# Kernel optimization log

Measured on AMD Instinct MI355X. Metric: run time of the kernel, lower is better.

## Reference

```python
import jax, jax.numpy as jnp
import numpy as np

K_BASE = 8
K_MAX = 20
NUM_GROUPS = 16  # min(32, 64 // 4)
EPS = 1e-5


def _knn_idx_adaptive(x, mask, k_base=K_BASE, k_max=K_MAX):
    # x: [B, N, D] float, mask: [B, N] bool. Returns idx: [B, N, k_max] int32.
    B, N, D = x.shape
    x2 = jnp.sum(x * x, axis=-1, keepdims=True)              # [B, N, 1]
    dist2 = x2 + x2.transpose(0, 2, 1) - 2.0 * jnp.einsum('bnd,bmd->bnm', x, x)
    dist2 = jnp.clip(dist2, 0.0)
    valid = mask[:, :, None] & mask[:, None, :]
    eye = jnp.eye(N, dtype=bool)[None]
    dist2 = jnp.where(valid & ~eye, dist2, jnp.inf)
    counts = mask.sum(axis=1)                                 # [B]
    k_per = jnp.clip(jnp.sqrt(counts.astype(jnp.float32) / 50.0) * k_base,
                     k_base, k_max).astype(jnp.int32)         # truncation == torch .long()
    k_global = jnp.minimum(k_max, jnp.maximum(1, counts.min() - 1))
    _, idx = jax.lax.top_k(-dist2, k_max)                     # [B, N, k_max]
    first_valid = jnp.argmax(mask, axis=1)                    # [B]
    cols = jnp.arange(k_max)[None, None, :]
    k_eff = jnp.minimum(k_per, k_global)[:, None, None]
    # cols < k_eff: true top-k neighbors; [k_eff, k_global): repeat first valid; >= k_global: pad 0
    idx = jnp.where(cols < k_eff, idx,
                    jnp.where(cols < k_global, first_valid[:, None, None], 0))
    return idx


def _group_norm(h, gamma, beta, num_groups=NUM_GROUPS, eps=EPS):
    # h: [..., C]
    shp = h.shape
    C = shp[-1]
    hg = h.reshape(shp[:-1] + (num_groups, C // num_groups))
    mu = hg.mean(axis=-1, keepdims=True)
    var = hg.var(axis=-1, keepdims=True)
    hg = (hg - mu) * jax.lax.rsqrt(var + eps)
    return hg.reshape(shp) * gamma + beta


def setup_inputs() -> dict:
    key = jax.random.key(0)
    kx, kl, k1, k2 = jax.random.split(key, 4)
    B, N, D, C = 16, 1024, 64, 64
    x = jax.random.normal(kx, (B, N, D), dtype=jnp.float32)
    lengths = jax.random.randint(kl, (B,), 256, N + 1)
    mask = jnp.arange(N)[None, :] < lengths[:, None]          # [B, N] bool
    W1 = jax.random.normal(k1, (2 * D, C), dtype=jnp.float32) / np.sqrt(2 * D)
    b1 = jnp.zeros((C,), dtype=jnp.float32)
    gamma = jnp.ones((C,), dtype=jnp.float32)
    beta = jnp.zeros((C,), dtype=jnp.float32)
    W2 = jax.random.normal(k2, (C, C), dtype=jnp.float32) / np.sqrt(C)
    b2 = jnp.zeros((C,), dtype=jnp.float32)
    return {"x": x, "mask": mask, "W1": W1, "b1": b1,
            "gamma": gamma, "beta": beta, "W2": W2, "b2": b2}


def reference(x, mask, W1, b1, gamma, beta, W2, b2):
    B, N, D = x.shape
    idx = _knn_idx_adaptive(x, mask)                          # [B, N, k]
    k = idx.shape[-1]
    x_nb = jnp.take_along_axis(x[:, :, None, :].repeat(1, axis=2),
                               idx[..., None], axis=1) if False else \
        x[jnp.arange(B)[:, None, None], idx]                  # [B, N, k, D]
    x_i = jnp.broadcast_to(x[:, :, None, :], (B, N, k, D))
    edge = jnp.concatenate([x_i, x_nb - x_i], axis=-1)        # [B, N, k, 2D]
    h = jax.nn.relu(_group_norm(edge @ W1 + b1, gamma, beta)) # [B, N, k, C]
    h = h @ W2 + b2
    out = h.max(axis=2)                                       # [B, N, C]
    return out * mask[..., None].astype(out.dtype)
```

## Files before the change

kernel.cpp:

```cpp
#include <hip/hip_runtime.h>
#include <stdint.h>

#define BB 16
#define NN 1024
#define DD 64
#define CC 64
#define KMAX 20
#define ROWS 8
#define PW 8

typedef unsigned long long u64;
typedef float f32x2 __attribute__((ext_vector_type(2)));
typedef float f32x4v __attribute__((ext_vector_type(4)));
typedef short bf16x8 __attribute__((ext_vector_type(8)));

__device__ inline u64 umin64(u64 a, u64 b) { return a < b ? a : b; }

__device__ inline u64 bitonic_sort64(u64 v, int lane) {
#pragma unroll
    for (int k = 2; k <= 64; k <<= 1) {
#pragma unroll
        for (int j = k >> 1; j > 0; j >>= 1) {
            u64 o = __shfl_xor(v, j);
            bool keepmin = (((lane & j) == 0) == ((lane & k) == 0));
            bool take = ((o < v) == keepmin);
            v = take ? o : v;
        }
    }
    return v;
}

__device__ inline unsigned f2bf(float f) {
    unsigned u = __float_as_uint(f);
    return (u + 0x7FFFu + ((u >> 16) & 1u)) >> 16;
}

__device__ inline bf16x8 pack8(const float4 a, const float4 b) {
    union { unsigned u[4]; bf16x8 v; } r;
    r.u[0] = f2bf(a.x) | (f2bf(a.y) << 16);
    r.u[1] = f2bf(a.z) | (f2bf(a.w) << 16);
    r.u[2] = f2bf(b.x) | (f2bf(b.y) << 16);
    r.u[3] = f2bf(b.z) | (f2bf(b.w) << 16);
    return r.v;
}

__device__ inline void gn4(float4& h, const float4 g, const float4 be) {
    float mu = (h.x + h.y + h.z + h.w) * 0.25f;
    float dx = h.x - mu, dy = h.y - mu, dz = h.z - mu, dw = h.w - mu;
    float var = (dx * dx + dy * dy + dz * dz + dw * dw) * 0.25f;
    float rs = __builtin_amdgcn_rsqf(var + 1e-5f);
    h.x = fmaxf(fmaf(dx * rs, g.x, be.x), 0.f);
    h.y = fmaxf(fmaf(dy * rs, g.y, be.y), 0.f);
    h.z = fmaxf(fmaf(dz * rs, g.z, be.z), 0.f);
    h.w = fmaxf(fmaf(dw * rs, g.w, be.w), 0.f);
}

__global__ __launch_bounds__(256) void k1_feats(const float* __restrict__ x,
                                                const float* __restrict__ W1,
                                                const float* __restrict__ b1,
                                                float* __restrict__ base,
                                                float* __restrict__ fb,
                                                float* __restrict__ x2,
                                                float* __restrict__ xT,
                                                const void* __restrict__ maskp,
                                                int* __restrict__ counts,
                                                int* __restrict__ keff) {
    __shared__ float sXT[32][65];
    __shared__ int scnt[BB];
    int w = threadIdx.x >> 6, lane = threadIdx.x & 63;
    int p0 = blockIdx.x * 32;
    int pw0 = p0 + w * PW;

    float w1a[DD], w1b[DD];
#pragma unroll
    for (int d = 0; d < DD; ++d) {
        w1a[d] = W1[d * CC + lane];
        w1b[d] = W1[(DD + d) * CC + lane];
    }
    float b1c = b1[lane];

#pragma unroll
    for (int q = 0; q < PW; ++q) {
        int p_s = __builtin_amdgcn_readfirstlane(pw0 + q);
        const float* xp = x + (size_t)p_s * DD;
        float xv = xp[lane];
        float sq = xv * xv;
        for (int off = 32; off; off >>= 1) sq += __shfl_xor(sq, off);
        if (lane == 0) x2[p_s] = sq;
        sXT[w * PW + q][lane] = xv;
        f32x2 acc2 = {0.f, 0.f};
#pragma unroll
        for (int d = 0; d < DD; ++d) {
            float xd = xp[d];
            acc2 = __builtin_elementwise_fma((f32x2){xd, xd},
                                             (f32x2){w1a[d], w1b[d]}, acc2);
        }
        base[(size_t)p_s * CC + lane] = acc2.x - acc2.y + b1c;
        fb[(size_t)p_s * CC + lane] = acc2.y;
    }
    __syncthreads();
    {
        int b = p0 >> 10, nb = p0 & 1023;
#pragma unroll
        for (int i = 0; i < 8; ++i) {
            int d = i * 8 + (threadIdx.x >> 5);
            int pt = threadIdx.x & 31;
            xT[(((size_t)(b << 6) + d) << 10) + nb + pt] = sXT[pt][d];
        }
    }

    if (blockIdx.x == 0) {
        const unsigned char* mb = (const unsigned char*)maskp;
        const int* mi = (const int*)maskp;
        bool bytelayout = (mb[1] != 0);
        for (int bq = 0; bq < 4; ++bq) {
            int bb = w * 4 + bq;
            int s = 0;
            for (int i = 0; i < 16; ++i) {
                int nn2 = lane + (i << 6);
                int v = bytelayout ? (mb[bb * NN + nn2] ? 1 : 0)
                                   : (mi[bb * NN + nn2] ? 1 : 0);
                s += v;
            }
            for (int off = 32; off; off >>= 1) s += __shfl_xor(s, off);
            if (lane == 0) scnt[bb] = s;
        }
        __syncthreads();
        int t = threadIdx.x;
        if (t < BB) {
            int minc = scnt[0];
            for (int qq = 1; qq < BB; ++qq) minc = min(minc, scnt[qq]);
            int kglob = min(KMAX, max(1, minc - 1));
            float c = (float)scnt[t];
            float v = sqrtf(c / 50.0f) * 8.0f;
            v = fminf(fmaxf(v, 8.0f), 20.0f);
            int kper = (int)v;
            counts[t] = scnt[t];
            keff[t] = min(kper, kglob);
        }
    }
}

#define CE(a, b)                                                      \
    {                                                                 \
        bool sw_ = pk[b] < pk[a];                                     \
        u64 ta_ = pk[a];                                              \
        pk[a] = sw_ ? pk[b] : pk[a];                                  \
        pk[b] = sw_ ? ta_ : pk[b];                                    \
    }

#define ROWFMA(r, rv, cv)                                                        \
    {                                                                            \
        axy[r] = __builtin_elementwise_fma((f32x2){rv, rv}, (f32x2){cv.x, cv.y}, \
                                           axy[r]);                              \
        azw[r] = __builtin_elementwise_fma((f32x2){rv, rv}, (f32x2){cv.z, cv.w}, \
                                           azw[r]);                              \
    }

__global__ __launch_bounds__(256) void k2_knn(const float* __restrict__ x,
                                              const float* __restrict__ xT,
                                              const float* __restrict__ x2,
                                              const int* __restrict__ counts,
                                              const int* __restrict__ keff,
                                              int* __restrict__ idx) {
    __shared__ float sD[ROWS][NN];
    __shared__ float sX2[NN];
    __shared__ u64 sSv[4][64];
    int b = blockIdx.x >> 7;
    int n0 = (blockIdx.x & 127) * ROWS;
    int cnt = counts[b];
    if (n0 >= cnt) return;
    int kef = keff[b];
    int w = threadIdx.x >> 6, lane = threadIdx.x & 63;
    int t = threadIdx.x;
    *(float4*)&sX2[t << 2] = *(const float4*)(x2 + (b << 10) + (t << 2));
    __syncthreads();

    if ((w << 8) < cnt) {
        f32x2 axy[ROWS], azw[ROWS];
#pragma unroll
        for (int r = 0; r < ROWS; ++r) { axy[r] = (f32x2){0.f, 0.f}; azw[r] = (f32x2){0.f, 0.f}; }
        const float* xTb = xT + ((size_t)b << 16);
        const float* xrow0 = x + ((size_t)(b << 10) + n0) * DD;
        int c0 = (w << 8) + (lane << 2);
        for (int d0 = 0; d0 < DD; d0 += 4) {
            float4 cv0 = *(const float4*)(xTb + ((size_t)(d0 + 0) << 10) + c0);
            float4 cv1 = *(const float4*)(xTb + ((size_t)(d0 + 1) << 10) + c0);
            float4 cv2 = *(const float4*)(xTb + ((size_t)(d0 + 2) << 10) + c0);
            float4 cv3 = *(const float4*)(xTb + ((size_t)(d0 + 3) << 10) + c0);
#pragma unroll
            for (int r = 0; r < ROWS; ++r) {
                float4 rv = *(const float4*)(xrow0 + r * DD + d0);
                ROWFMA(r, rv.x, cv0)
                ROWFMA(r, rv.y, cv1)
                ROWFMA(r, rv.z, cv2)
                ROWFMA(r, rv.w, cv3)
            }
        }
#pragma unroll
        for (int r = 0; r < ROWS; ++r)
            *(float4*)&sD[r][c0] = make_float4(axy[r].x, axy[r].y, azw[r].x, azw[r].y);
    }
    __syncthreads();

    for (int rr = 0; rr < 2; ++rr) {
        int r = w + rr * 4;
        int n = n0 + r;
        if (n >= cnt) continue;
        float x2n = sX2[n];
        u64 pk[16];
#pragma unroll
        for (int tt = 0; tt < 16; ++tt) {
            int c = (tt << 6) + lane;
            float dot = sD[r][c];
            float dd = fmaxf((x2n + sX2[c]) - 2.0f * dot, 0.0f);
            pk[tt] = (c < cnt && c != n)
                ? (((u64)__float_as_uint(dd) << 32) | (unsigned)c)
                : ~0ULL;
        }
        u64 h01 = umin64(pk[0], pk[1]),   h23 = umin64(pk[2], pk[3]);
        u64 h45 = umin64(pk[4], pk[5]),   h67 = umin64(pk[6], pk[7]);
        u64 h89 = umin64(pk[8], pk[9]),   hab = umin64(pk[10], pk[11]);
        u64 hcd = umin64(pk[12], pk[13]), hef = umin64(pk[14], pk[15]);
        u64 h = umin64(umin64(umin64(h01, h23), umin64(h45, h67)),
                       umin64(umin64(h89, hab), umin64(hcd, hef)));
        unsigned h32 = (unsigned)(h >> 32);
        unsigned prefix = 0u;
        int rank = kef;
#pragma unroll
        for (int bbit = 31; bbit >= 0; --bbit) {
            unsigned bitm = 1u << bbit;
            bool cand0 = ((((u64)(h32 ^ prefix)) >> (bbit + 1)) == 0) &&
                         ((h32 & bitm) == 0);
            u64 m0 = __ballot(cand0);
            int c0 = __popcll(m0);
            if (rank > c0) { rank -= c0; prefix |= bitm; }
        }
        u64 t0 = (((u64)prefix) << 32) | 0xFFFFFFFFULL;
        int cle = 0;
#pragma unroll
        for (int i = 0; i < 16; ++i) cle += (pk[i] <= t0) ? 1 : 0;
        int incl = cle;
#pragma unroll
        for (int off = 1; off < 64; off <<= 1) {
            int o = __shfl_up(incl, off);
            incl += (lane >= off) ? o : 0;
        }
        int S = __shfl(incl, 63);
        size_t prow = (size_t)(b << 10) + n;
        if (S <= 64) {
            int pos = incl - cle;
#pragma unroll
            for (int i = 0; i < 16; ++i) {
                if (pk[i] <= t0) { sSv[w][pos] = pk[i]; ++pos; }
            }
            u64 sv = (lane < S) ? sSv[w][lane] : ~0ULL;
            sv = bitonic_sort64(sv, lane);
            if (lane < KMAX)
                idx[prow * KMAX + lane] = (lane < kef) ? (int)(unsigned)(sv & 0xffffffffu) : 0;
        } else {
            CE(0,1) CE(2,3) CE(4,5) CE(6,7) CE(8,9) CE(10,11) CE(12,13) CE(14,15)
            CE(0,2) CE(1,3) CE(4,6) CE(5,7) CE(8,10) CE(9,11) CE(12,14) CE(13,15)
            CE(1,2) CE(5,6) CE(9,10) CE(13,14)
            CE(0,4) CE(1,5) CE(2,6) CE(3,7) CE(8,12) CE(9,13) CE(10,14) CE(11,15)
            CE(2,4) CE(3,5) CE(10,12) CE(11,13)
            CE(1,2) CE(3,4) CE(5,6) CE(9,10) CE(11,12) CE(13,14)
            CE(0,8) CE(1,9) CE(2,10) CE(3,11) CE(4,12) CE(5,13) CE(6,14) CE(7,15)
            CE(4,8) CE(5,9) CE(6,10) CE(7,11)
            CE(2,4) CE(3,5) CE(6,8) CE(7,9) CE(10,12) CE(11,13)
            CE(1,2) CE(3,4) CE(5,6) CE(7,8) CE(9,10) CE(11,12) CE(13,14)
            u64 myhead = pk[0];
            int my_m = 0;
            for (int j = 0; j < kef; ++j) {
                u64 g = myhead;
                for (int off = 32; off; off >>= 1) {
                    u64 o = __shfl_xor(g, off);
                    g = (o < g) ? o : g;
                }
                my_m = (j == lane) ? (int)(unsigned)(g & 0xffffffffu) : my_m;
                bool win = (myhead == g);
#pragma unroll
                for (int tt = 0; tt < 15; ++tt) pk[tt] = win ? pk[tt + 1] : pk[tt];
                pk[15] = win ? ~0ULL : pk[15];
                myhead = pk[0];
            }
            if (lane < KMAX)
                idx[prow * KMAX + lane] = (lane < kef) ? my_m : 0;
        }
    }
}

__global__ __launch_bounds__(256, 2) void k3_mlp(const float* __restrict__ base,
                                                 const float* __restrict__ fb,
                                                 const int* __restrict__ idx,
                                                 const int* __restrict__ counts,
                                                 const float* __restrict__ gamma,
                                                 const float* __restrict__ beta,
                                                 const float* __restrict__ W2,
                                                 const float* __restrict__ b2,
                                                 float* __restrict__ out) {
    __shared__ float sC[4][64][20];
    int w = threadIdx.x >> 6, lane = threadIdx.x & 63;
    int lg = lane >> 4, lr = lane & 15;
    int p0 = blockIdx.x * 16;
    int b = p0 >> 10;
    int n0b = p0 & 1023;
    int cnt = counts[b];
    int pt = p0 + lr;
    bool aval = (n0b + lr) < cnt;

    bf16x8 Bf[4][2];
#pragma unroll
    for (int nt = 0; nt < 4; ++nt)
#pragma unroll
        for (int kt = 0; kt < 2; ++kt) {
            float4 lo, hi;
            const float* wp = W2 + (size_t)(kt * 32 + lg * 8) * CC + nt * 16 + lr;
            lo.x = wp[0 * CC]; lo.y = wp[1 * CC]; lo.z = wp[2 * CC]; lo.w = wp[3 * CC];
            hi.x = wp[4 * CC]; hi.y = wp[5 * CC]; hi.z = wp[6 * CC]; hi.w = wp[7 * CC];
            Bf[nt][kt] = pack8(lo, hi);
        }

    const float* bp = base + (size_t)pt * CC + lg * 8;
    float4 baA0 = *(const float4*)(bp);
    float4 baA1 = *(const float4*)(bp + 4);
    float4 baB0 = *(const float4*)(bp + 32);
    float4 baB1 = *(const float4*)(bp + 36);
    const float* gp = gamma + lg * 8;
    float4 gA0 = *(const float4*)(gp),      gA1 = *(const float4*)(gp + 4);
    float4 gB0 = *(const float4*)(gp + 32), gB1 = *(const float4*)(gp + 36);
    const float* bep = beta + lg * 8;
    float4 eA0 = *(const float4*)(bep),      eA1 = *(const float4*)(bep + 4);
    float4 eB0 = *(const float4*)(bep + 32), eB1 = *(const float4*)(bep + 36);

    const float* fbb = fb + ((size_t)(b << 10)) * CC;
    const int* idxp = idx + (size_t)pt * KMAX;

    f32x4v cmax[4];
#pragma unroll
    for (int nt = 0; nt < 4; ++nt) cmax[nt] = (f32x4v){-1e30f, -1e30f, -1e30f, -1e30f};

#pragma unroll
    for (int jj = 0; jj < 5; ++jj) {
        int j = w * 5 + jj;
        int m = aval ? idxp[j] : 0;
        const float* fr = fbb + (size_t)m * CC + lg * 8;
        float4 hA0 = *(const float4*)(fr);
        float4 hA1 = *(const float4*)(fr + 4);
        float4 hB0 = *(const float4*)(fr + 32);
        float4 hB1 = *(const float4*)(fr + 36);
        hA0.x += baA0.x; hA0.y += baA0.y; hA0.z += baA0.z; hA0.w += baA0.w;
        hA1.x += baA1.x; hA1.y += baA1.y; hA1.z += baA1.z; hA1.w += baA1.w;
        hB0.x += baB0.x; hB0.y += baB0.y; hB0.z += baB0.z; hB0.w += baB0.w;
        hB1.x += baB1.x; hB1.y += baB1.y; hB1.z += baB1.z; hB1.w += baB1.w;
        gn4(hA0, gA0, eA0);
        gn4(hA1, gA1, eA1);
        gn4(hB0, gB0, eB0);
        gn4(hB1, gB1, eB1);
        bf16x8 A0 = pack8(hA0, hA1);
        bf16x8 A1 = pack8(hB0, hB1);
#pragma unroll
        for (int nt = 0; nt < 4; ++nt) {
            f32x4v c = {0.f, 0.f, 0.f, 0.f};
            c = __builtin_amdgcn_mfma_f32_16x16x32_bf16(A0, Bf[nt][0], c, 0, 0, 0);
            c = __builtin_amdgcn_mfma_f32_16x16x32_bf16(A1, Bf[nt][1], c, 0, 0, 0);
            cmax[nt].x = fmaxf(cmax[nt].x, c.x);
            cmax[nt].y = fmaxf(cmax[nt].y, c.y);
            cmax[nt].z = fmaxf(cmax[nt].z, c.z);
            cmax[nt].w = fmaxf(cmax[nt].w, c.w);
        }
    }
#pragma unroll
    for (int nt = 0; nt < 4; ++nt)
        *(float4*)&sC[w][lane][nt * 4] = (float4){cmax[nt].x, cmax[nt].y, cmax[nt].z, cmax[nt].w};
    __syncthreads();
    float b2c = b2[lane];
#pragma unroll
    for (int q = 0; q < 4; ++q) {
        int R = w * 4 + q;
        int src = ((R >> 2) << 4) + lr;
        int reg = (lg << 2) + (R & 3);
        float v = fmaxf(fmaxf(sC[0][src][reg], sC[1][src][reg]),
                        fmaxf(sC[2][src][reg], sC[3][src][reg]));
        bool valid = (n0b + R) < cnt;
        out[(size_t)(p0 + R) * CC + lane] = valid ? (v + b2c) : 0.f;
    }
}

extern "C" void kernel_launch(void* const* d_in, const int* in_sizes, int n_in,
                              void* d_out, int out_size, void* d_ws, size_t ws_size,
                              hipStream_t stream) {
    const float* x     = (const float*)d_in[0];
    const void*  maskp = d_in[1];
    const float* W1    = (const float*)d_in[2];
    const float* b1    = (const float*)d_in[3];
    const float* gamma = (const float*)d_in[4];
    const float* beta  = (const float*)d_in[5];
    const float* W2    = (const float*)d_in[6];
    const float* b2    = (const float*)d_in[7];
    float* out = (float*)d_out;

    int* d_counts = (int*)d_ws;
    int* d_keff   = d_counts + 16;
    float* d_x2   = (float*)(d_counts + 32);
    float* d_base = d_x2 + BB * NN;
    float* d_fb   = d_base + (size_t)BB * NN * CC;
    int* d_idx    = (int*)(d_fb + (size_t)BB * NN * CC);
    float* d_xT   = (float*)d_out;

    hipLaunchKernelGGL(k1_feats, dim3(BB * NN / 32), dim3(256), 0, stream,
                       x, W1, b1, d_base, d_fb, d_x2, d_xT, maskp, d_counts, d_keff);
    hipLaunchKernelGGL(k2_knn, dim3(BB * (NN / ROWS)), dim3(256), 0, stream,
                       x, d_xT, d_x2, d_counts, d_keff, d_idx);
    hipLaunchKernelGGL(k3_mlp, dim3(BB * NN / 16), dim3(256), 0, stream,
                       d_base, d_fb, d_idx, d_counts, gamma, beta, W2, b2, out);
}
```

Baseline: 96.30 us.

## Use split-bf16 MFMA for edge features and interleave two kNN rows per wave

The per-point feature projection in k1 is rewritten to use 16x16x32 bf16 MFMA with a hi/lo split (three products) to keep close to fp32 accuracy. Each block now covers 64 points and the transpose store uses float4 writes. In k2 each wave handles its two rows together, with interleaved radix-select ballots, prefix scans and bitonic sorts to expose more ILP, and it reuses the sD rows as scratch for compaction. This raises register pressure, and the split-bf16 approximation can shift results slightly.

```diff
diff --git a/kernel.cpp b/kernel.cpp
--- a/kernel.cpp
+++ b/kernel.cpp
@@ -7,7 +7,6 @@
 #define CC 64
 #define KMAX 20
 #define ROWS 8
-#define PW 8
 
 typedef unsigned long long u64;
 typedef float f32x2 __attribute__((ext_vector_type(2)));
@@ -15,20 +14,6 @@
 typedef short bf16x8 __attribute__((ext_vector_type(8)));
 
 __device__ inline u64 umin64(u64 a, u64 b) { return a < b ? a : b; }
-
-__device__ inline u64 bitonic_sort64(u64 v, int lane) {
-#pragma unroll
-    for (int k = 2; k <= 64; k <<= 1) {
-#pragma unroll
-        for (int j = k >> 1; j > 0; j >>= 1) {
-            u64 o = __shfl_xor(v, j);
-            bool keepmin = (((lane & j) == 0) == ((lane & k) == 0));
-            bool take = ((o < v) == keepmin);
-            v = take ? o : v;
-        }
-    }
-    return v;
-}
 
 __device__ inline unsigned f2bf(float f) {
     unsigned u = __float_as_uint(f);
@@ -42,6 +27,20 @@
     r.u[2] = f2bf(b.x) | (f2bf(b.y) << 16);
     r.u[3] = f2bf(b.z) | (f2bf(b.w) << 16);
     return r.v;
+}
+
+struct bfpair { bf16x8 hi, lo; };
+__device__ __forceinline__ bfpair split8(const float v[8]) {
+    union { unsigned u[4]; bf16x8 x; } H, L;
+#pragma unroll
+    for (int i = 0; i < 4; ++i) {
+        unsigned h0 = f2bf(v[2 * i]), h1 = f2bf(v[2 * i + 1]);
+        float r0 = v[2 * i] - __uint_as_float(h0 << 16);
+        float r1 = v[2 * i + 1] - __uint_as_float(h1 << 16);
+        H.u[i] = h0 | (h1 << 16);
+        L.u[i] = f2bf(r0) | (f2bf(r1) << 16);
+    }
+    bfpair r; r.hi = H.x; r.lo = L.x; return r;
 }
 
 __device__ inline void gn4(float4& h, const float4 g, const float4 be) {
@@ -65,47 +64,84 @@
                                                 const void* __restrict__ maskp,
                                                 int* __restrict__ counts,
                                                 int* __restrict__ keff) {
-    __shared__ float sXT[32][65];
+    __shared__ float sXT[64][65];
     __shared__ int scnt[BB];
     int w = threadIdx.x >> 6, lane = threadIdx.x & 63;
-    int p0 = blockIdx.x * 32;
-    int pw0 = p0 + w * PW;
-
-    float w1a[DD], w1b[DD];
-#pragma unroll
-    for (int d = 0; d < DD; ++d) {
-        w1a[d] = W1[d * CC + lane];
-        w1b[d] = W1[(DD + d) * CC + lane];
-    }
-    float b1c = b1[lane];
-
-#pragma unroll
-    for (int q = 0; q < PW; ++q) {
-        int p_s = __builtin_amdgcn_readfirstlane(pw0 + q);
-        const float* xp = x + (size_t)p_s * DD;
-        float xv = xp[lane];
+    int lg = lane >> 4, lr = lane & 15;
+    int p0 = blockIdx.x * 64;
+    int pw0 = p0 + w * 16;
+
+    float av[8];
+    bfpair A[2];
+    {
+        const float* xr = x + (size_t)(pw0 + lr) * DD;
+#pragma unroll
+        for (int kt = 0; kt < 2; ++kt) {
+            float4 a0 = *(const float4*)(xr + kt * 32 + lg * 8);
+            float4 a1 = *(const float4*)(xr + kt * 32 + lg * 8 + 4);
+            av[0] = a0.x; av[1] = a0.y; av[2] = a0.z; av[3] = a0.w;
+            av[4] = a1.x; av[5] = a1.y; av[6] = a1.z; av[7] = a1.w;
+            A[kt] = split8(av);
+        }
+    }
+    bfpair Wa[4][2], Wb[4][2];
+#pragma unroll
+    for (int nt = 0; nt < 4; ++nt)
+#pragma unroll
+        for (int kt = 0; kt < 2; ++kt) {
+            const float* wpa = W1 + (size_t)(kt * 32 + lg * 8) * CC + nt * 16 + lr;
+            float wv[8];
+#pragma unroll
+            for (int e = 0; e < 8; ++e) wv[e] = wpa[e * CC];
+            Wa[nt][kt] = split8(wv);
+            const float* wpb = wpa + (size_t)DD * CC;
+#pragma unroll
+            for (int e = 0; e < 8; ++e) wv[e] = wpb[e * CC];
+            Wb[nt][kt] = split8(wv);
+        }
+
+    f32x4v P[4], Q[4];
+#pragma unroll
+    for (int nt = 0; nt < 4; ++nt) { P[nt] = (f32x4v){0,0,0,0}; Q[nt] = (f32x4v){0,0,0,0}; }
+#pragma unroll
+    for (int nt = 0; nt < 4; ++nt)
+#pragma unroll
+        for (int kt = 0; kt < 2; ++kt) {
+            P[nt] = __builtin_amdgcn_mfma_f32_16x16x32_bf16(A[kt].hi, Wa[nt][kt].hi, P[nt], 0, 0, 0);
+            P[nt] = __builtin_amdgcn_mfma_f32_16x16x32_bf16(A[kt].hi, Wa[nt][kt].lo, P[nt], 0, 0, 0);
+            P[nt] = __builtin_amdgcn_mfma_f32_16x16x32_bf16(A[kt].lo, Wa[nt][kt].hi, P[nt], 0, 0, 0);
+            Q[nt] = __builtin_amdgcn_mfma_f32_16x16x32_bf16(A[kt].hi, Wb[nt][kt].hi, Q[nt], 0, 0, 0);
+            Q[nt] = __builtin_amdgcn_mfma_f32_16x16x32_bf16(A[kt].hi, Wb[nt][kt].lo, Q[nt], 0, 0, 0);
+            Q[nt] = __builtin_amdgcn_mfma_f32_16x16x32_bf16(A[kt].lo, Wb[nt][kt].hi, Q[nt], 0, 0, 0);
+        }
+#pragma unroll
+    for (int nt = 0; nt < 4; ++nt) {
+        float b1c = b1[nt * 16 + lr];
+#pragma unroll
+        for (int r = 0; r < 4; ++r) {
+            size_t off = (size_t)(pw0 + lg * 4 + r) * CC + nt * 16 + lr;
+            base[off] = P[nt][r] - Q[nt][r] + b1c;
+            fb[off] = Q[nt][r];
+        }
+    }
+
+    for (int q = 0; q < 16; ++q) {
+        int p = pw0 + q;
+        float xv = x[(size_t)p * DD + lane];
+        sXT[w * 16 + q][lane] = xv;
         float sq = xv * xv;
         for (int off = 32; off; off >>= 1) sq += __shfl_xor(sq, off);
-        if (lane == 0) x2[p_s] = sq;
-        sXT[w * PW + q][lane] = xv;
-        f32x2 acc2 = {0.f, 0.f};
-#pragma unroll
-        for (int d = 0; d < DD; ++d) {
-            float xd = xp[d];
-            acc2 = __builtin_elementwise_fma((f32x2){xd, xd},
-                                             (f32x2){w1a[d], w1b[d]}, acc2);
-        }
-        base[(size_t)p_s * CC + lane] = acc2.x - acc2.y + b1c;
-        fb[(size_t)p_s * CC + lane] = acc2.y;
+        if (lane == 0) x2[p] = sq;
     }
     __syncthreads();
     {
         int b = p0 >> 10, nb = p0 & 1023;
 #pragma unroll
-        for (int i = 0; i < 8; ++i) {
-            int d = i * 8 + (threadIdx.x >> 5);
-            int pt = threadIdx.x & 31;
-            xT[(((size_t)(b << 6) + d) << 10) + nb + pt] = sXT[pt][d];
+        for (int i = 0; i < 4; ++i) {
+            int d = i * 16 + (threadIdx.x >> 4);
+            int pt4 = (threadIdx.x & 15) << 2;
+            float4 vv = {sXT[pt4][d], sXT[pt4 + 1][d], sXT[pt4 + 2][d], sXT[pt4 + 3][d]};
+            *(float4*)&xT[(((size_t)(b << 6) + d) << 10) + nb + pt4] = vv;
         }
     }
 
@@ -149,6 +185,58 @@
         pk[b] = sw_ ? ta_ : pk[b];                                    \
     }
 
+__device__ __forceinline__ u64 head16(const u64 (&pk)[16]) {
+    u64 h01 = umin64(pk[0], pk[1]),   h23 = umin64(pk[2], pk[3]);
+    u64 h45 = umin64(pk[4], pk[5]),   h67 = umin64(pk[6], pk[7]);
+    u64 h89 = umin64(pk[8], pk[9]),   hab = umin64(pk[10], pk[11]);
+    u64 hcd = umin64(pk[12], pk[13]), hef = umin64(pk[14], pk[15]);
+    return umin64(umin64(umin64(h01, h23), umin64(h45, h67)),
+                  umin64(umin64(h89, hab), umin64(hcd, hef)));
+}
+
+__device__ __forceinline__ int sortpop(u64 (&pk)[16], int kef, int lane) {
+    CE(0,1) CE(2,3) CE(4,5) CE(6,7) CE(8,9) CE(10,11) CE(12,13) CE(14,15)
+    CE(0,2) CE(1,3) CE(4,6) CE(5,7) CE(8,10) CE(9,11) CE(12,14) CE(13,15)
+    CE(1,2) CE(5,6) CE(9,10) CE(13,14)
+    CE(0,4) CE(1,5) CE(2,6) CE(3,7) CE(8,12) CE(9,13) CE(10,14) CE(11,15)
+    CE(2,4) CE(3,5) CE(10,12) CE(11,13)
+    CE(1,2) CE(3,4) CE(5,6) CE(9,10) CE(11,12) CE(13,14)
+    CE(0,8) CE(1,9) CE(2,10) CE(3,11) CE(4,12) CE(5,13) CE(6,14) CE(7,15)
+    CE(4,8) CE(5,9) CE(6,10) CE(7,11)
+    CE(2,4) CE(3,5) CE(6,8) CE(7,9) CE(10,12) CE(11,13)
+    CE(1,2) CE(3,4) CE(5,6) CE(7,8) CE(9,10) CE(11,12) CE(13,14)
+    u64 myhead = pk[0];
+    int my_m = 0;
+    for (int j = 0; j < kef; ++j) {
+        u64 g = myhead;
+        for (int off = 32; off; off >>= 1) {
+            u64 o = __shfl_xor(g, off);
+            g = (o < g) ? o : g;
+        }
+        my_m = (j == lane) ? (int)(unsigned)(g & 0xffffffffu) : my_m;
+        bool win = (myhead == g);
+#pragma unroll
+        for (int tt = 0; tt < 15; ++tt) pk[tt] = win ? pk[tt + 1] : pk[tt];
+        pk[15] = win ? ~0ULL : pk[15];
+        myhead = pk[0];
+    }
+    return my_m;
+}
+
+__device__ __forceinline__ void bitonic_x2(u64& a, u64& b, int lane) {
+#pragma unroll
+    for (int k = 2; k <= 64; k <<= 1) {
+#pragma unroll
+        for (int j = k >> 1; j > 0; j >>= 1) {
+            u64 oa = __shfl_xor(a, j);
+            u64 ob = __shfl_xor(b, j);
+            bool keepmin = (((lane & j) == 0) == ((lane & k) == 0));
+            a = ((oa < a) == keepmin) ? oa : a;
+            b = ((ob < b) == keepmin) ? ob : b;
+        }
+    }
+}
+
 #define ROWFMA(r, rv, cv)                                                        \
     {                                                                            \
         axy[r] = __builtin_elementwise_fma((f32x2){rv, rv}, (f32x2){cv.x, cv.y}, \
@@ -165,7 +253,6 @@
                                               int* __restrict__ idx) {
     __shared__ float sD[ROWS][NN];
     __shared__ float sX2[NN];
-    __shared__ u64 sSv[4][64];
     int b = blockIdx.x >> 7;
     int n0 = (blockIdx.x & 127) * ROWS;
     int cnt = counts[b];
@@ -203,89 +290,80 @@
     }
     __syncthreads();
 
-    for (int rr = 0; rr < 2; ++rr) {
-        int r = w + rr * 4;
-        int n = n0 + r;
-        if (n >= cnt) continue;
-        float x2n = sX2[n];
-        u64 pk[16];
-#pragma unroll
-        for (int tt = 0; tt < 16; ++tt) {
-            int c = (tt << 6) + lane;
-            float dot = sD[r][c];
-            float dd = fmaxf((x2n + sX2[c]) - 2.0f * dot, 0.0f);
-            pk[tt] = (c < cnt && c != n)
-                ? (((u64)__float_as_uint(dd) << 32) | (unsigned)c)
-                : ~0ULL;
-        }
-        u64 h01 = umin64(pk[0], pk[1]),   h23 = umin64(pk[2], pk[3]);
-        u64 h45 = umin64(pk[4], pk[5]),   h67 = umin64(pk[6], pk[7]);
-        u64 h89 = umin64(pk[8], pk[9]),   hab = umin64(pk[10], pk[11]);
-        u64 hcd = umin64(pk[12], pk[13]), hef = umin64(pk[14], pk[15]);
-        u64 h = umin64(umin64(umin64(h01, h23), umin64(h45, h67)),
-                       umin64(umin64(h89, hab), umin64(hcd, hef)));
-        unsigned h32 = (unsigned)(h >> 32);
-        unsigned prefix = 0u;
-        int rank = kef;
-#pragma unroll
-        for (int bbit = 31; bbit >= 0; --bbit) {
-            unsigned bitm = 1u << bbit;
-            bool cand0 = ((((u64)(h32 ^ prefix)) >> (bbit + 1)) == 0) &&
-                         ((h32 & bitm) == 0);
-            u64 m0 = __ballot(cand0);
-            int c0 = __popcll(m0);
-            if (rank > c0) { rank -= c0; prefix |= bitm; }
-        }
-        u64 t0 = (((u64)prefix) << 32) | 0xFFFFFFFFULL;
-        int cle = 0;
-#pragma unroll
-        for (int i = 0; i < 16; ++i) cle += (pk[i] <= t0) ? 1 : 0;
-        int incl = cle;
-#pragma unroll
-        for (int off = 1; off < 64; off <<= 1) {
-            int o = __shfl_up(incl, off);
-            incl += (lane >= off) ? o : 0;
-        }
-        int S = __shfl(incl, 63);
-        size_t prow = (size_t)(b << 10) + n;
-        if (S <= 64) {
-            int pos = incl - cle;
-#pragma unroll
-            for (int i = 0; i < 16; ++i) {
-                if (pk[i] <= t0) { sSv[w][pos] = pk[i]; ++pos; }
-            }
-            u64 sv = (lane < S) ? sSv[w][lane] : ~0ULL;
-            sv = bitonic_sort64(sv, lane);
-            if (lane < KMAX)
-                idx[prow * KMAX + lane] = (lane < kef) ? (int)(unsigned)(sv & 0xffffffffu) : 0;
-        } else {
-            CE(0,1) CE(2,3) CE(4,5) CE(6,7) CE(8,9) CE(10,11) CE(12,13) CE(14,15)
-            CE(0,2) CE(1,3) CE(4,6) CE(5,7) CE(8,10) CE(9,11) CE(12,14) CE(13,15)
-            CE(1,2) CE(5,6) CE(9,10) CE(13,14)
-            CE(0,4) CE(1,5) CE(2,6) CE(3,7) CE(8,12) CE(9,13) CE(10,14) CE(11,15)
-            CE(2,4) CE(3,5) CE(10,12) CE(11,13)
-            CE(1,2) CE(3,4) CE(5,6) CE(9,10) CE(11,12) CE(13,14)
-            CE(0,8) CE(1,9) CE(2,10) CE(3,11) CE(4,12) CE(5,13) CE(6,14) CE(7,15)
-            CE(4,8) CE(5,9) CE(6,10) CE(7,11)
-            CE(2,4) CE(3,5) CE(6,8) CE(7,9) CE(10,12) CE(11,13)
-            CE(1,2) CE(3,4) CE(5,6) CE(7,8) CE(9,10) CE(11,12) CE(13,14)
-            u64 myhead = pk[0];
-            int my_m = 0;
-            for (int j = 0; j < kef; ++j) {
-                u64 g = myhead;
-                for (int off = 32; off; off >>= 1) {
-                    u64 o = __shfl_xor(g, off);
-                    g = (o < g) ? o : g;
-                }
-                my_m = (j == lane) ? (int)(unsigned)(g & 0xffffffffu) : my_m;
-                bool win = (myhead == g);
-#pragma unroll
-                for (int tt = 0; tt < 15; ++tt) pk[tt] = win ? pk[tt + 1] : pk[tt];
-                pk[15] = win ? ~0ULL : pk[15];
-                myhead = pk[0];
-            }
-            if (lane < KMAX)
-                idx[prow * KMAX + lane] = (lane < kef) ? my_m : 0;
+    int rA = w, rB = w + 4;
+    int nA = n0 + rA, nB = n0 + rB;
+    bool vA = nA < cnt, vB = nB < cnt;
+    if (!vA) return;
+    float x2A = sX2[nA];
+    float x2B = sX2[nB & 1023];
+    u64 pkA[16], pkB[16];
+#pragma unroll
+    for (int tt = 0; tt < 16; ++tt) {
+        int c = (tt << 6) + lane;
+        float dA = fmaxf((x2A + sX2[c]) - 2.0f * sD[rA][c], 0.0f);
+        float dB = fmaxf((x2B + sX2[c]) - 2.0f * sD[rB][c], 0.0f);
+        pkA[tt] = (c < cnt && c != nA)
+            ? (((u64)__float_as_uint(dA) << 32) | (unsigned)c) : ~0ULL;
+        pkB[tt] = (vB && c < cnt && c != nB)
+            ? (((u64)__float_as_uint(dB) << 32) | (unsigned)c) : ~0ULL;
+    }
+    u64 hA = head16(pkA), hB = head16(pkB);
+    unsigned hA32 = (unsigned)(hA >> 32), hB32 = (unsigned)(hB >> 32);
+    unsigned prefA = 0u, prefB = 0u;
+    int rankA = kef, rankB = kef;
+#pragma unroll
+    for (int bbit = 31; bbit >= 0; --bbit) {
+        unsigned bitm = 1u << bbit;
+        bool cA = ((((u64)(hA32 ^ prefA)) >> (bbit + 1)) == 0) && ((hA32 & bitm) == 0);
+        bool cB = ((((u64)(hB32 ^ prefB)) >> (bbit + 1)) == 0) && ((hB32 & bitm) == 0);
+        u64 mA = __ballot(cA);
+        u64 mB = __ballot(cB);
+        int nA0 = __popcll(mA), nB0 = __popcll(mB);
+        if (rankA > nA0) { rankA -= nA0; prefA |= bitm; }
+        if (rankB > nB0) { rankB -= nB0; prefB |= bitm; }
+    }
+    u64 t0A = (((u64)prefA) << 32) | 0xFFFFFFFFULL;
+    u64 t0B = vB ? ((((u64)prefB) << 32) | 0xFFFFFFFFULL) : 0ULL;
+    int cleA = 0, cleB = 0;
+#pragma unroll
+    for (int i = 0; i < 16; ++i) {
+        cleA += (pkA[i] <= t0A) ? 1 : 0;
+        cleB += (pkB[i] <= t0B) ? 1 : 0;
+    }
+    int incA = cleA, incB = cleB;
+#pragma unroll
+    for (int off = 1; off < 64; off <<= 1) {
+        int oA = __shfl_up(incA, off);
+        int oB = __shfl_up(incB, off);
+        incA += (lane >= off) ? oA : 0;
+        incB += (lane >= off) ? oB : 0;
+    }
+    int SA = __shfl(incA, 63), SB = __shfl(incB, 63);
+    size_t prowA = (size_t)(b << 10) + nA;
+    size_t prowB = (size_t)(b << 10) + nB;
+    if (SA <= 64 && SB <= 64) {
+        u64* svA = (u64*)&sD[rA][0];
+        u64* svB = (u64*)&sD[rB][0];
+        int pA = incA - cleA, pB = incB - cleB;
+#pragma unroll
+        for (int i = 0; i < 16; ++i) {
+            if (pkA[i] <= t0A) { svA[pA] = pkA[i]; ++pA; }
+            if (pkB[i] <= t0B) { svB[pB] = pkB[i]; ++pB; }
+        }
+        u64 sA = (lane < SA) ? svA[lane] : ~0ULL;
+        u64 sB = (lane < SB) ? svB[lane] : ~0ULL;
+        bitonic_x2(sA, sB, lane);
+        if (lane < KMAX) {
+            idx[prowA * KMAX + lane] = (lane < kef) ? (int)(unsigned)(sA & 0xffffffffu) : 0;
+            if (vB)
+                idx[prowB * KMAX + lane] = (lane < kef) ? (int)(unsigned)(sB & 0xffffffffu) : 0;
+        }
+    } else {
+        int mA = sortpop(pkA, kef, lane);
+        if (lane < KMAX) idx[prowA * KMAX + lane] = (lane < kef) ? mA : 0;
+        if (vB) {
+            int mB = sortpop(pkB, kef, lane);
+            if (lane < KMAX) idx[prowB * KMAX + lane] = (lane < kef) ? mB : 0;
         }
     }
 }
@@ -408,7 +486,7 @@
     int* d_idx    = (int*)(d_fb + (size_t)BB * NN * CC);
     float* d_xT   = (float*)d_out;
 
-    hipLaunchKernelGGL(k1_feats, dim3(BB * NN / 32), dim3(256), 0, stream,
+    hipLaunchKernelGGL(k1_feats, dim3(BB * NN / 64), dim3(256), 0, stream,
                        x, W1, b1, d_base, d_fb, d_x2, d_xT, maskp, d_counts, d_keff);
     hipLaunchKernelGGL(k2_knn, dim3(BB * (NN / ROWS)), dim3(256), 0, stream,
                        x, d_xT, d_x2, d_counts, d_keff, d_idx);
```

New measurement: 97.48 us. No clear change (+1.2%).
